# Kernel tuning notes

Measured on AMD Instinct MI355X. Metric: run time of the kernel, lower is better.

## Reference

```python
import jax, jax.numpy as jnp
import numpy as np
from jax import lax

BATCH, C, HH, WW = 4, 3, 512, 512


def _dark_min(x, patch):
    # min over channels, reflect-pad, min over patch x patch window (torch unfold+min)
    pad = (patch - 1) // 2
    m = jnp.min(x, axis=1, keepdims=True)                      # [B,1,H,W]
    m = jnp.pad(m, ((0, 0), (0, 0), (pad, pad), (pad, pad)), mode='reflect')
    return lax.reduce_window(m, jnp.array(jnp.inf, m.dtype), lax.min,
                             (1, 1, patch, patch), (1, 1, 1, 1), 'VALID')


def _soft_thresh(x, lam):
    return jnp.sign(x) * jnp.maximum(jnp.abs(x) - lam, 0.0)


def _conv3x3(x, w):
    return lax.conv_general_dilated(x, w, (1, 1), 'SAME',
                                    dimension_numbers=('NCHW', 'OIHW', 'NCHW'))


def setup_inputs() -> dict:
    key = jax.random.key(0)
    names = ['I', 't_p', 'B_p', 'B', 't', 'J', 'G', 'H', 'P', 'Q', 'u', 'v', 'X', 'Y']
    keys = jax.random.split(key, len(names) + 2)
    inp = {n: jax.random.uniform(keys[i], (BATCH, C, HH, WW), dtype=jnp.float32)
           for i, n in enumerate(names)}
    for g in ['gamma_1', 'gamma_2', 'gamma_3', 'gamma_4', 'gamma_5']:
        inp[g] = jnp.array([3.001], dtype=jnp.float32)
    inp['t1d_w'] = jax.random.normal(keys[-2], (1, 3, 1, 1), dtype=jnp.float32) * 0.3
    inp['hnet_w'] = jax.random.normal(keys[-1], (3, 3, 3, 3), dtype=jnp.float32) * 0.1
    inp['patch_size'] = 35
    return inp


def _forward(I, t_p, B_p, B, t, J, G, H, P, Q, u, v, X, Y,
             gamma_1, gamma_2, gamma_3, gamma_4, gamma_5, t1d_w, hnet_w, patch_size):
    lam1, lam2, lam3, lam4, lam5 = 1.0, 0.7, 0.3, 1.0, 1.0

    # ---- get_mean_value + mapping_index (vectorized over batch) ----
    mean = jnp.mean(J, axis=(2, 3))                 # [B,3]
    idx = jnp.argsort(mean, axis=1)                 # ascending, like torch.sort
    ms = jnp.take_along_axis(mean, idx, axis=1)     # sorted means
    gather = lambda k: jnp.take_along_axis(J, idx[:, k][:, None, None, None], axis=1)
    J_l, J_m, J_s = gather(2), gather(1), gather(0)           # [B,1,H,W]
    bar = lambda k: ms[:, k][:, None, None, None]
    J_m = J_m + (bar(2) - bar(1)) * J_l
    J_s = J_s + (bar(2) - bar(0)) * J_l
    ch = jnp.arange(3)[None, :]                     # scatter channels back
    J = jnp.where((ch == idx[:, 1:2])[:, :, None, None], J_m, J)
    J = jnp.where((ch == idx[:, 0:1])[:, :, None, None], J_s, J)

    # ---- B update (spatial mean broadcast back) ----
    Bn = (lam3 * B_p - lam1 * (J * t - I) * (1.0 - t)) / (lam1 * (1.0 - t) ** 2 + lam3)
    Bn = jnp.mean(Bn, axis=(2, 3), keepdims=True) * jnp.ones_like(I)

    # ---- t update + 1x1 conv + channel replicate ----
    tn = (lam2 * t_p + gamma_4 * H - lam1 * (Bn - I) * (J - Bn) - X) / \
         (lam1 * (J - Bn) ** 2 + lam2 + gamma_4)
    t1 = jnp.einsum('oc,bchw->bohw', t1d_w[:, :, 0, 0], tn)   # [B,1,H,W]
    tn = jnp.concatenate([t1, t1, t1], axis=1)

    # ---- J, u, v updates ----
    Jn = (lam1 * (tn * (I - Bn * (1.0 - tn))) + gamma_3 * G + gamma_4 * u
          - gamma_5 * v - Y + gamma_5) / (lam1 * tn * tn + gamma_3 + gamma_4 + gamma_5)
    un = (gamma_1 * u + gamma_4 * Jn) / (gamma_1 + gamma_4)
    vn = (gamma_2 * v - gamma_5 * Jn + gamma_5) / (gamma_2 + gamma_5)

    # ---- H_Net (conv stand-in for RDN), dual updates ----
    Hn = _conv3x3(tn + X / gamma_4, hnet_w)
    Xn = X + gamma_4 * (tn - Hn)
    Yn = Y + gamma_3 * (Jn - G)

    # ---- dark channel + soft threshold ----
    M_u = _dark_min(un, patch_size)
    M_v = _dark_min(vn, patch_size)
    Pn = _soft_thresh(M_u, lam4 / gamma_1)
    Qn = _soft_thresh(M_v, lam5 / gamma_1)

    return (Bn, tn, Jn, G, Hn, Pn, Qn, un, vn, Xn, Yn, gamma_3)


def reference(I, t_p, B_p, B, t, J, G, H, P, Q, u, v, X, Y,
              gamma_1, gamma_2, gamma_3, gamma_4, gamma_5, t1d_w, hnet_w, patch_size):
    return _forward(I, t_p, B_p, B, t, J, G, H, P, Q, u, v, X, Y,
                    gamma_1, gamma_2, gamma_3, gamma_4, gamma_5, t1d_w, hnet_w, patch_size)
```

## Files before the change

### kernel.cpp

```cpp
#include <hip/hip_runtime.h>
#include <math.h>

#define W_ 512
#define H_ 512
#define HW_ 262144
#define HW4_ 65536
#define CHW_ 786432

#define O_Bn 0
#define O_tn 3145728
#define O_Jn 6291456
#define O_G  9437184
#define O_Hn 12582912
#define O_Pn 15728640
#define O_Qn 16777216
#define O_un 17825792
#define O_vn 20971520
#define O_Xn 24117248
#define O_Yn 27262976
#define O_g3 30408704

#define LAM2 0.7f
#define LAM3 0.3f

#define WS_SUMS   0
#define WS_ALPHA  8192
#define WS_IDX2   8204
#define WS_BNS    8208
#define WS_SCR    16384

typedef float nfloat4 __attribute__((ext_vector_type(4)));

__device__ __forceinline__ void nt_store4(float4 v, float4* p) {
    nfloat4 nv; nv.x = v.x; nv.y = v.y; nv.z = v.z; nv.w = v.w;
    __builtin_nontemporal_store(nv, (nfloat4*)p);
}

__global__ __launch_bounds__(256) void kRed(const float* __restrict__ J,
                                            const float* __restrict__ tt,
                                            const float* __restrict__ B_p,
                                            const float* __restrict__ I,
                                            float* __restrict__ sums) {
    int blk = blockIdx.x;
    int b = blk >> 7, chunk = blk & 127;
    size_t pb = (size_t)b * (CHW_ / 4);
    size_t cb = (size_t)chunk * 512;
    const float4* J4 = (const float4*)J;
    const float4* t4 = (const float4*)tt;
    const float4* B4 = (const float4*)B_p;
    const float4* I4 = (const float4*)I;

    float aJ[3] = {0.f, 0.f, 0.f};
    float a1[3] = {0.f, 0.f, 0.f};
    float a2[9] = {0.f, 0.f, 0.f, 0.f, 0.f, 0.f, 0.f, 0.f, 0.f};

    #pragma unroll
    for (int k = 0; k < 2; ++k) {
        size_t o = cb + threadIdx.x + k * 256;
        float4 j0 = J4[pb + 0 * HW4_ + o];
        float4 j1 = J4[pb + 1 * HW4_ + o];
        float4 j2 = J4[pb + 2 * HW4_ + o];
        #pragma unroll
        for (int c = 0; c < 3; ++c) {
            float4 tv = t4[pb + (size_t)c * HW4_ + o];
            float4 bp = B4[pb + (size_t)c * HW4_ + o];
            float4 iv = I4[pb + (size_t)c * HW4_ + o];
            float4 jc = (c == 0) ? j0 : (c == 1 ? j1 : j2);
#define REDC(m) { \
            float omt = 1.f - tv.m; \
            float r = 1.f / (omt * omt + LAM3); \
            float g = tv.m * omt * r; \
            aJ[c] += jc.m; \
            a1[c] += (LAM3 * bp.m - (jc.m * tv.m - iv.m) * omt) * r; \
            a2[0 * 3 + c] += j0.m * g; \
            a2[1 * 3 + c] += j1.m * g; \
            a2[2 * 3 + c] += j2.m * g; }
            REDC(x) REDC(y) REDC(z) REDC(w)
#undef REDC
        }
    }

    float vals[15];
    #pragma unroll
    for (int c = 0; c < 3; ++c) { vals[c] = aJ[c]; vals[3 + c] = a1[c]; }
    #pragma unroll
    for (int s = 0; s < 9; ++s) vals[6 + s] = a2[s];

    __shared__ float lds[4][15];
    int lane = threadIdx.x & 63, w = threadIdx.x >> 6;
    #pragma unroll
    for (int s = 0; s < 15; ++s) {
        float v = vals[s];
        #pragma unroll
        for (int off = 32; off; off >>= 1) v += __shfl_down(v, off, 64);
        if (lane == 0) lds[w][s] = v;
    }
    __syncthreads();
    if (threadIdx.x < 15) {
        int s = threadIdx.x;
        sums[blk * 16 + s] = lds[0][s] + lds[1][s] + lds[2][s] + lds[3][s];
    }
}

__global__ __launch_bounds__(256) void kFin(const float* __restrict__ sums,
                     float* __restrict__ alpha, int* __restrict__ idx2,
                     float* __restrict__ BnS,
                     const float* __restrict__ g3p, float* __restrict__ outg3) {
    __shared__ float part[64][4];
    __shared__ float tot[4][15];
    int t = threadIdx.x;
    int g = t >> 2, sub = t & 3;
    if (g < 60) {
        int b = g / 15, s = g % 15;
        const float* p = sums + (size_t)b * 128 * 16 + s;
        float acc = 0.f;
        #pragma unroll 8
        for (int ch = sub; ch < 128; ch += 4) acc += p[ch * 16];
        part[g][sub] = acc;
    }
    __syncthreads();
    if (t < 60) {
        tot[t / 15][t % 15] = (part[t][0] + part[t][1]) + (part[t][2] + part[t][3]);
    }
    __syncthreads();
    if (t < 4) {
        const float invHW = 1.0f / (float)HW_;
        float m[3] = {tot[t][0] * invHW, tot[t][1] * invHW, tot[t][2] * invHW};
        int r[3];
        #pragma unroll
        for (int i = 0; i < 3; ++i) {
            int ri = 0;
            #pragma unroll
            for (int j = 0; j < 3; ++j)
                if (j != i && (m[j] < m[i] || (m[j] == m[i] && j < i))) ri++;
            r[i] = ri;
        }
        int idx[3]; float ms[3];
        #pragma unroll
        for (int i = 0; i < 3; ++i) { idx[r[i]] = i; ms[r[i]] = m[i]; }
        idx2[t] = idx[2];
        float a[3] = {0.f, 0.f, 0.f};
        a[idx[1]] = ms[2] - ms[1];
        a[idx[0]] = ms[2] - ms[0];
        #pragma unroll
        for (int c = 0; c < 3; ++c) {
            alpha[t * 3 + c] = a[c];
            BnS[t * 3 + c] = (tot[t][3 + c] - a[c] * tot[t][6 + idx[2] * 3 + c]) * invHW;
        }
    }
    if (t == 0) *outg3 = g3p[0];
}

__global__ __launch_bounds__(256) void kMain(
    const float* __restrict__ I, const float* __restrict__ t_p,
    const float* __restrict__ Hm, const float* __restrict__ Xm,
    const float* __restrict__ J, const float* __restrict__ u,
    const float* __restrict__ v, const float* __restrict__ Y,
    const float* __restrict__ G,
    const float* __restrict__ g1p, const float* __restrict__ g2p,
    const float* __restrict__ g3p, const float* __restrict__ g4p,
    const float* __restrict__ g5p, const float* __restrict__ t1w,
    const float* __restrict__ alpha, const int* __restrict__ idx2,
    const float* __restrict__ BnS,
    float* __restrict__ out)
{
    int id = blockIdx.x * 256 + threadIdx.x;
    int b = id >> 16, q = id & (HW4_ - 1);
    float g1 = g1p[0], g2 = g2p[0], g3 = g3p[0], g4 = g4p[0], g5 = g5p[0];
    float wc[3] = {t1w[0], t1w[1], t1w[2]};
    int i2 = idx2[b];
    size_t pb = (size_t)b * (CHW_ / 4);
    const float4* I4p = (const float4*)I;
    const float4* tp4p = (const float4*)t_p;
    const float4* H4p = (const float4*)Hm;
    const float4* X4p = (const float4*)Xm;
    const float4* J4p = (const float4*)J;
    const float4* u4p = (const float4*)u;
    const float4* v4p = (const float4*)v;
    const float4* Y4p = (const float4*)Y;
    const float4* G4p = (const float4*)G;
    float4* o4 = (float4*)out;

    float4 Jl = J4p[pb + (size_t)i2 * HW4_ + q];
    float4 t1 = make_float4(0.f, 0.f, 0.f, 0.f);
    float4 Isv[3]; float Bsv[3];
    const float den2 = LAM2 + g4;
    #pragma unroll
    for (int c = 0; c < 3; ++c) {
        size_t o = pb + (size_t)c * HW4_ + q;
        float4 I4 = I4p[o], tp4 = tp4p[o], H4 = H4p[o], X4 = X4p[o], Jv = J4p[o];
        float al = alpha[b * 3 + c], Bnv = BnS[b * 3 + c];
        float wcc = wc[c];
#define STEP1(m) { \
        float d_ = (Jv.m + al * Jl.m) - Bnv; \
        float tnr_ = (LAM2 * tp4.m + g4 * H4.m - (Bnv - I4.m) * d_ - X4.m) / (d_ * d_ + den2); \
        t1.m += wcc * tnr_; }
        STEP1(x) STEP1(y) STEP1(z) STEP1(w)
#undef STEP1
        Isv[c] = I4; Bsv[c] = Bnv;
    }
    float g345 = g3 + g4 + g5;
    float4 invDen;
    invDen.x = 1.f / (t1.x * t1.x + g345);
    invDen.y = 1.f / (t1.y * t1.y + g345);
    invDen.z = 1.f / (t1.z * t1.z + g345);
    invDen.w = 1.f / (t1.w * t1.w + g345);
    float invDu = 1.f / (g1 + g4), invDv = 1.f / (g2 + g5);
    float4 cu = make_float4(1e30f, 1e30f, 1e30f, 1e30f);
    float4 cv = cu;
    #pragma unroll
    for (int c = 0; c < 3; ++c) {
        size_t o = pb + (size_t)c * HW4_ + q;
        float4 u4 = u4p[o], v4 = v4p[o], Y4 = Y4p[o], G4 = G4p[o];
        float Bnv = Bsv[c];
        float4 Jn4, un4, vn4, Yn4;
#define STEP2(m) { \
        float Jn_ = (t1.m * (Isv[c].m - Bnv * (1.f - t1.m)) + g3 * G4.m + g4 * u4.m \
                     - g5 * v4.m - Y4.m + g5) * invDen.m; \
        float un_ = (g1 * u4.m + g4 * Jn_) * invDu; \
        float vn_ = (g2 * v4.m - g5 * Jn_ + g5) * invDv; \
        Jn4.m = Jn_; un4.m = un_; vn4.m = vn_; \
        Yn4.m = Y4.m + g3 * (Jn_ - G4.m); \
        cu.m = fminf(cu.m, un_); cv.m = fminf(cv.m, vn_); }
        STEP2(x) STEP2(y) STEP2(z) STEP2(w)
#undef STEP2
        nt_store4(make_float4(Bnv, Bnv, Bnv, Bnv), &o4[O_Bn / 4 + o]);
        o4[O_tn / 4 + o] = t1;
        nt_store4(Jn4, &o4[O_Jn / 4 + o]);
        nt_store4(G4,  &o4[O_G  / 4 + o]);
        nt_store4(un4, &o4[O_un / 4 + o]);
        nt_store4(vn4, &o4[O_vn / 4 + o]);
        nt_store4(Yn4, &o4[O_Yn / 4 + o]);
    }
    o4[O_Pn / 4 + (size_t)b * HW4_ + q] = cu;
    o4[O_Qn / 4 + (size_t)b * HW4_ + q] = cv;
}

__global__ __launch_bounds__(256) void kHMin(const float* __restrict__ out,
                                             float* __restrict__ scr) {
    __shared__ float row[546];
    int blk = blockIdx.x;
    int tensor = blk >> 11;
    int rem = blk & 2047;
    int b = rem >> 9, y = rem & 511;
    const float* src = out + (tensor ? O_Qn : O_Pn) + b * HW_ + y * W_;
    float* dst = scr + (size_t)(tensor * 4 + b) * HW_ + y * W_;
    for (int j = threadIdx.x; j < 546; j += 256) {
        int xx = j - 17;
        xx = xx < 0 ? -xx : (xx >= W_ ? 2 * W_ - 2 - xx : xx);
        row[j] = src[xx];
    }
    __syncthreads();
    for (int x = threadIdx.x; x < W_; x += 256) {
        float m = row[x];
        #pragma unroll
        for (int k = 1; k < 35; ++k) m = fminf(m, row[x + k]);
        dst[x] = m;
    }
}

__global__ __launch_bounds__(256) void kTail(const float* __restrict__ scr,
                                             const float* __restrict__ Xm,
                                             const float* __restrict__ hw,
                                             const float* __restrict__ g1p,
                                             const float* __restrict__ g4p,
                                             float* __restrict__ out) {
    __shared__ float w[81];
    if (blockIdx.x < 8192) {
        int tensor = blockIdx.x >> 12;
        int lid = ((blockIdx.x & 4095) << 8) + threadIdx.x;
        int b = lid >> 18, p = lid & (HW_ - 1);
        int y = p >> 9, x = p & 511;
        const float* R = scr + (size_t)(tensor * 4 + b) * HW_;
        float m = 1e30f;
        #pragma unroll
        for (int k = 0; k < 35; ++k) {
            int yy = y + k - 17;
            yy = yy < 0 ? -yy : (yy >= H_ ? 2 * H_ - 2 - yy : yy);
            m = fminf(m, R[yy * W_ + x]);
        }
        float lam = 1.0f / g1p[0];
        float s = (m > 0.f) ? 1.f : (m < 0.f ? -1.f : 0.f);
        float r = s * fmaxf(fabsf(m) - lam, 0.f);
        __builtin_nontemporal_store(r, &out[(tensor ? O_Qn : O_Pn) + b * HW_ + p]);
    } else {
        if (threadIdx.x < 81) w[threadIdx.x] = hw[threadIdx.x];
        __syncthreads();
        int id = (blockIdx.x - 8192) * 256 + threadIdx.x;
        int b = id >> 18, p = id & (HW_ - 1);
        int y = p >> 9, x = p & 511;
        float g4 = g4p[0], ig4 = 1.f / g4;
        const float* tn = out + O_tn + (size_t)b * CHW_;
        float acc0 = 0.f, acc1 = 0.f, acc2 = 0.f;
        #pragma unroll
        for (int ky = 0; ky < 3; ++ky) {
            int yy = y + ky - 1;
            if (yy < 0 || yy >= H_) continue;
            #pragma unroll
            for (int kx = 0; kx < 3; ++kx) {
                int xx = x + kx - 1;
                if (xx < 0 || xx >= W_) continue;
                int pp = yy * W_ + xx;
                float t1v = tn[pp];
                #pragma unroll
                for (int i = 0; i < 3; ++i) {
                    float Av = t1v + Xm[(size_t)(b * 3 + i) * HW_ + pp] * ig4;
                    int kk = i * 9 + ky * 3 + kx;
                    acc0 += w[kk] * Av;
                    acc1 += w[27 + kk] * Av;
                    acc2 += w[54 + kk] * Av;
                }
            }
        }
        float t1c = tn[p];
        float acc[3] = {acc0, acc1, acc2};
        #pragma unroll
        for (int o = 0; o < 3; ++o) {
            size_t oo = (size_t)(b * 3 + o) * HW_ + p;
            __builtin_nontemporal_store(acc[o], &out[O_Hn + oo]);
            __builtin_nontemporal_store(Xm[oo] + g4 * (t1c - acc[o]), &out[O_Xn + oo]);
        }
    }
}

extern "C" void kernel_launch(void* const* d_in, const int* in_sizes, int n_in,
                              void* d_out, int out_size, void* d_ws, size_t ws_size,
                              hipStream_t stream) {
    (void)in_sizes; (void)n_in; (void)out_size; (void)ws_size;
    const float* I   = (const float*)d_in[0];
    const float* t_p = (const float*)d_in[1];
    const float* B_p = (const float*)d_in[2];
    const float* tt  = (const float*)d_in[4];
    const float* J   = (const float*)d_in[5];
    const float* G   = (const float*)d_in[6];
    const float* Hm  = (const float*)d_in[7];
    const float* u   = (const float*)d_in[10];
    const float* v   = (const float*)d_in[11];
    const float* X   = (const float*)d_in[12];
    const float* Y   = (const float*)d_in[13];
    const float* g1  = (const float*)d_in[14];
    const float* g2  = (const float*)d_in[15];
    const float* g3  = (const float*)d_in[16];
    const float* g4  = (const float*)d_in[17];
    const float* g5  = (const float*)d_in[18];
    const float* t1w = (const float*)d_in[19];
    const float* hw  = (const float*)d_in[20];
    float* out = (float*)d_out;
    float* ws  = (float*)d_ws;

    float* sums  = ws + WS_SUMS;
    float* alpha = ws + WS_ALPHA;
    int*   idx2  = (int*)(ws + WS_IDX2);
    float* BnS   = ws + WS_BNS;
    float* scr   = ws + WS_SCR;

    kRed<<<512, 256, 0, stream>>>(J, tt, B_p, I, sums);
    kFin<<<1, 256, 0, stream>>>(sums, alpha, idx2, BnS, g3, out + O_g3);
    kMain<<<1024, 256, 0, stream>>>(I, t_p, Hm, X, J, u, v, Y, G,
                                    g1, g2, g3, g4, g5, t1w, alpha, idx2, BnS, out);
    kHMin<<<4096, 256, 0, stream>>>(out, scr);
    kTail<<<12288, 256, 0, stream>>>(scr, X, hw, g1, g4, out);
}
```

Before: 322.7 us.

## Fuse horizontal min into main kernel and tile 3x3 conv through LDS

Folds the horizontal 35-wide min pass into kMain: each block writes its two rows of channel-min values to shared memory, fills in the reflect padding and writes horizontal mins straight to scratch. This removes the kHMin launch and the write and re-read of the unfiltered Pn/Qn values. The tail kernel now does the vertical min with float4 loads, and computes the 3x3 conv from an LDS tile of (tn + X/g4) rows shared across output channels. Xn is rewritten as g4*(A - Hn), which is algebraically equal to the original. A leftover dead kTail stub remains in the source, and the kMain fusion assumes each 256-thread block covers exactly two full image rows.

```diff
diff --git a/kernel.cpp b/kernel.cpp
--- a/kernel.cpp
+++ b/kernel.cpp
@@ -162,8 +162,10 @@
     const float* __restrict__ g5p, const float* __restrict__ t1w,
     const float* __restrict__ alpha, const int* __restrict__ idx2,
     const float* __restrict__ BnS,
-    float* __restrict__ out)
+    float* __restrict__ out, float* __restrict__ scr)
 {
+    __shared__ float pad[2][2][560];
+
     int id = blockIdx.x * 256 + threadIdx.x;
     int b = id >> 16, q = id & (HW4_ - 1);
     float g1 = g1p[0], g2 = g2p[0], g3 = g3p[0], g4 = g4p[0], g5 = g5p[0];
@@ -232,93 +234,206 @@
         nt_store4(vn4, &o4[O_vn / 4 + o]);
         nt_store4(Yn4, &o4[O_Yn / 4 + o]);
     }
-    o4[O_Pn / 4 + (size_t)b * HW4_ + q] = cu;
-    o4[O_Qn / 4 + (size_t)b * HW4_ + q] = cv;
-}
-
-__global__ __launch_bounds__(256) void kHMin(const float* __restrict__ out,
-                                             float* __restrict__ scr) {
-    __shared__ float row[546];
-    int blk = blockIdx.x;
-    int tensor = blk >> 11;
-    int rem = blk & 2047;
-    int b = rem >> 9, y = rem & 511;
-    const float* src = out + (tensor ? O_Qn : O_Pn) + b * HW_ + y * W_;
-    float* dst = scr + (size_t)(tensor * 4 + b) * HW_ + y * W_;
-    for (int j = threadIdx.x; j < 546; j += 256) {
-        int xx = j - 17;
-        xx = xx < 0 ? -xx : (xx >= W_ ? 2 * W_ - 2 - xx : xx);
-        row[j] = src[xx];
-    }
+
+    int t = threadIdx.x;
+    int rrow = t >> 7;
+    int x0 = (t & 127) * 4;
+    pad[0][rrow][17 + x0 + 0] = cu.x;
+    pad[0][rrow][17 + x0 + 1] = cu.y;
+    pad[0][rrow][17 + x0 + 2] = cu.z;
+    pad[0][rrow][17 + x0 + 3] = cu.w;
+    pad[1][rrow][17 + x0 + 0] = cv.x;
+    pad[1][rrow][17 + x0 + 1] = cv.y;
+    pad[1][rrow][17 + x0 + 2] = cv.z;
+    pad[1][rrow][17 + x0 + 3] = cv.w;
     __syncthreads();
-    for (int x = threadIdx.x; x < W_; x += 256) {
-        float m = row[x];
-        #pragma unroll
-        for (int k = 1; k < 35; ++k) m = fminf(m, row[x + k]);
-        dst[x] = m;
+    if (t < 136) {
+        int which = t / 34, e = t % 34;
+        int tens = which >> 1, rw = which & 1;
+        int j   = (e < 17) ? e : (529 + (e - 17));
+        int src = (e < 17) ? (34 - j) : (1056 - j);
+        pad[tens][rw][j] = pad[tens][rw][src];
+    }
+    __syncthreads();
+
+    int y0b = (blockIdx.x & 255) * 2;
+    int yg = y0b + rrow;
+    #pragma unroll
+    for (int tens = 0; tens < 2; ++tens) {
+        const float* rowp = &pad[tens][rrow][0];
+        const float4* rp4 = (const float4*)(rowp + x0);
+        float4 qv = rp4[0];
+        float a0 = qv.x, a1 = qv.y, a2 = qv.z;
+        float mc = qv.w;
+        #pragma unroll
+        for (int i = 1; i < 8; ++i) {
+            qv = rp4[i];
+            mc = fminf(mc, fminf(fminf(qv.x, qv.y), fminf(qv.z, qv.w)));
+        }
+        qv = rp4[8];
+        mc = fminf(mc, fminf(qv.x, fminf(qv.y, qv.z)));
+        float a35 = qv.w;
+        qv = rp4[9];
+        float a36 = qv.x, a37 = qv.y;
+        float4 r;
+        r.x = fminf(fminf(a0, a1), fminf(a2, mc));
+        r.y = fminf(fminf(a1, a2), fminf(mc, a35));
+        r.z = fminf(fminf(a2, mc), fminf(a35, a36));
+        r.w = fminf(fminf(mc, a35), fminf(a36, a37));
+        *(float4*)(scr + (size_t)(tens * 4 + b) * HW_ + yg * W_ + x0) = r;
     }
 }
 
 __global__ __launch_bounds__(256) void kTail(const float* __restrict__ scr,
-                                             const float* __restrict__ Xm,
                                              const float* __restrict__ hw,
                                              const float* __restrict__ g1p,
                                              const float* __restrict__ g4p,
                                              float* __restrict__ out) {
-    __shared__ float w[81];
-    if (blockIdx.x < 8192) {
-        int tensor = blockIdx.x >> 12;
-        int lid = ((blockIdx.x & 4095) << 8) + threadIdx.x;
-        int b = lid >> 18, p = lid & (HW_ - 1);
-        int y = p >> 9, x = p & 511;
+    __shared__ float A_lds[3][4][528];
+    __shared__ float wsh[81];
+    int t = threadIdx.x;
+
+    if (blockIdx.x < 2048) {
+        int tensor = blockIdx.x >> 10;
+        int lid = ((blockIdx.x & 1023) << 8) + t;
+        int b = lid >> 16, qq = lid & (HW4_ - 1);
+        int y = qq >> 7, xq = (qq & 127) << 2;
         const float* R = scr + (size_t)(tensor * 4 + b) * HW_;
-        float m = 1e30f;
+        float4 m = make_float4(1e30f, 1e30f, 1e30f, 1e30f);
         #pragma unroll
         for (int k = 0; k < 35; ++k) {
             int yy = y + k - 17;
             yy = yy < 0 ? -yy : (yy >= H_ ? 2 * H_ - 2 - yy : yy);
-            m = fminf(m, R[yy * W_ + x]);
+            float4 r4 = *(const float4*)(R + yy * W_ + xq);
+            m.x = fminf(m.x, r4.x); m.y = fminf(m.y, r4.y);
+            m.z = fminf(m.z, r4.z); m.w = fminf(m.w, r4.w);
         }
         float lam = 1.0f / g1p[0];
-        float s = (m > 0.f) ? 1.f : (m < 0.f ? -1.f : 0.f);
-        float r = s * fmaxf(fabsf(m) - lam, 0.f);
-        __builtin_nontemporal_store(r, &out[(tensor ? O_Qn : O_Pn) + b * HW_ + p]);
+        float4 r;
+#define SOFT(m_, r_) { float s = (m_ > 0.f) ? 1.f : (m_ < 0.f ? -1.f : 0.f); \
+                       r_ = s * fmaxf(fabsf(m_) - lam, 0.f); }
+        SOFT(m.x, r.x) SOFT(m.y, r.y) SOFT(m.z, r.z) SOFT(m.w, r.w)
+#undef SOFT
+        nt_store4(r, (float4*)(out + (tensor ? O_Qn : O_Pn) + b * HW_ + y * W_ + xq));
     } else {
-        if (threadIdx.x < 81) w[threadIdx.x] = hw[threadIdx.x];
+        int cblk = blockIdx.x - 2048;
+        int b = cblk >> 8;
+        int y0 = (cblk & 255) * 2;
+        float g4 = g4p[0], ig4 = 1.f / g4;
+        const float* tn0 = out + O_tn + (size_t)b * CHW_;
+        const float* Xb  = out + O_Xn;
+        (void)Xb;
+        if (t < 81) wsh[t] = hw[t];
+        #pragma unroll
+        for (int k = 0; k < 6; ++k) {
+            int g = t + 256 * k;
+            int i = g >> 9, r = (g >> 7) & 3, xq = (g & 127) << 2;
+            int yy = y0 - 1 + r;
+            float4 A4;
+            if (yy >= 0 && yy < H_) {
+                const float* Xrow =  nullptr;
+                (void)Xrow;
+                A4 = make_float4(0.f, 0.f, 0.f, 0.f);
+            }
+            (void)A4; (void)i; (void)r; (void)xq; (void)yy;
+        }
+    }
+}
+
+__global__ __launch_bounds__(256) void kTail2(const float* __restrict__ scr,
+                                              const float* __restrict__ Xm,
+                                              const float* __restrict__ hw,
+                                              const float* __restrict__ g1p,
+                                              const float* __restrict__ g4p,
+                                              float* __restrict__ out) {
+    __shared__ float A_lds[3][4][528];
+    __shared__ float wsh[81];
+    int t = threadIdx.x;
+
+    if (blockIdx.x < 2048) {
+        int tensor = blockIdx.x >> 10;
+        int lid = ((blockIdx.x & 1023) << 8) + t;
+        int b = lid >> 16, qq = lid & (HW4_ - 1);
+        int y = qq >> 7, xq = (qq & 127) << 2;
+        const float* R = scr + (size_t)(tensor * 4 + b) * HW_;
+        float4 m = make_float4(1e30f, 1e30f, 1e30f, 1e30f);
+        #pragma unroll
+        for (int k = 0; k < 35; ++k) {
+            int yy = y + k - 17;
+            yy = yy < 0 ? -yy : (yy >= H_ ? 2 * H_ - 2 - yy : yy);
+            float4 r4 = *(const float4*)(R + yy * W_ + xq);
+            m.x = fminf(m.x, r4.x); m.y = fminf(m.y, r4.y);
+            m.z = fminf(m.z, r4.z); m.w = fminf(m.w, r4.w);
+        }
+        float lam = 1.0f / g1p[0];
+        float4 r;
+#define SOFT(m_, r_) { float s = (m_ > 0.f) ? 1.f : (m_ < 0.f ? -1.f : 0.f); \
+                       r_ = s * fmaxf(fabsf(m_) - lam, 0.f); }
+        SOFT(m.x, r.x) SOFT(m.y, r.y) SOFT(m.z, r.z) SOFT(m.w, r.w)
+#undef SOFT
+        nt_store4(r, (float4*)(out + (tensor ? O_Qn : O_Pn) + b * HW_ + y * W_ + xq));
+    } else {
+        int cblk = blockIdx.x - 2048;
+        int b = cblk >> 8;
+        int y0 = (cblk & 255) * 2;
+        float g4 = g4p[0], ig4 = 1.f / g4;
+        const float* tn0 = out + O_tn + (size_t)b * CHW_;
+        if (t < 81) wsh[t] = hw[t];
+        #pragma unroll
+        for (int k = 0; k < 6; ++k) {
+            int g = t + 256 * k;
+            int i = g >> 9, r = (g >> 7) & 3, xq = (g & 127) << 2;
+            int yy = y0 - 1 + r;
+            float4 A4 = make_float4(0.f, 0.f, 0.f, 0.f);
+            if (yy >= 0 && yy < H_) {
+                float4 tn4 = *(const float4*)(tn0 + yy * W_ + xq);
+                float4 X4  = *(const float4*)(Xm + (size_t)(b * 3 + i) * HW_ + yy * W_ + xq);
+                A4.x = tn4.x + X4.x * ig4; A4.y = tn4.y + X4.y * ig4;
+                A4.z = tn4.z + X4.z * ig4; A4.w = tn4.w + X4.w * ig4;
+            }
+            *(float4*)(&A_lds[i][r][4 + xq]) = A4;
+        }
+        if (t < 24) {
+            int pair = t >> 1, side = t & 1;
+            A_lds[pair >> 2][pair & 3][side ? 516 : 3] = 0.f;
+        }
         __syncthreads();
-        int id = (blockIdx.x - 8192) * 256 + threadIdx.x;
-        int b = id >> 18, p = id & (HW_ - 1);
-        int y = p >> 9, x = p & 511;
-        float g4 = g4p[0], ig4 = 1.f / g4;
-        const float* tn = out + O_tn + (size_t)b * CHW_;
-        float acc0 = 0.f, acc1 = 0.f, acc2 = 0.f;
-        #pragma unroll
-        for (int ky = 0; ky < 3; ++ky) {
-            int yy = y + ky - 1;
-            if (yy < 0 || yy >= H_) continue;
+
+        int tl = t & 127, r_out = t >> 7;
+        float acc[3][4] = {{0.f,0.f,0.f,0.f},{0.f,0.f,0.f,0.f},{0.f,0.f,0.f,0.f}};
+        #pragma unroll
+        for (int i = 0; i < 3; ++i) {
             #pragma unroll
-            for (int kx = 0; kx < 3; ++kx) {
-                int xx = x + kx - 1;
-                if (xx < 0 || xx >= W_) continue;
-                int pp = yy * W_ + xx;
-                float t1v = tn[pp];
+            for (int ky = 0; ky < 3; ++ky) {
+                const float* Ar = &A_lds[i][r_out + ky][0];
+                const float* wp0 = &wsh[0 * 27 + i * 9 + ky * 3];
+                const float* wp1 = &wsh[1 * 27 + i * 9 + ky * 3];
+                const float* wp2 = &wsh[2 * 27 + i * 9 + ky * 3];
+                float w00 = wp0[0], w01 = wp0[1], w02 = wp0[2];
+                float w10 = wp1[0], w11 = wp1[1], w12 = wp1[2];
+                float w20 = wp2[0], w21 = wp2[1], w22 = wp2[2];
                 #pragma unroll
-                for (int i = 0; i < 3; ++i) {
-                    float Av = t1v + Xm[(size_t)(b * 3 + i) * HW_ + pp] * ig4;
-                    int kk = i * 9 + ky * 3 + kx;
-                    acc0 += w[kk] * Av;
-                    acc1 += w[27 + kk] * Av;
-                    acc2 += w[54 + kk] * Av;
+                for (int j = 0; j < 4; ++j) {
+                    int x = tl + 128 * j;
+                    float am = Ar[3 + x], a0 = Ar[4 + x], ap = Ar[5 + x];
+                    acc[0][j] += w00 * am + w01 * a0 + w02 * ap;
+                    acc[1][j] += w10 * am + w11 * a0 + w12 * ap;
+                    acc[2][j] += w20 * am + w21 * a0 + w22 * ap;
                 }
             }
         }
-        float t1c = tn[p];
-        float acc[3] = {acc0, acc1, acc2};
+        int yg = y0 + r_out;
         #pragma unroll
         for (int o = 0; o < 3; ++o) {
-            size_t oo = (size_t)(b * 3 + o) * HW_ + p;
-            __builtin_nontemporal_store(acc[o], &out[O_Hn + oo]);
-            __builtin_nontemporal_store(Xm[oo] + g4 * (t1c - acc[o]), &out[O_Xn + oo]);
+            #pragma unroll
+            for (int j = 0; j < 4; ++j) {
+                int x = tl + 128 * j;
+                size_t oo = (size_t)(b * 3 + o) * HW_ + yg * W_ + x;
+                float hn = acc[o][j];
+                float Ac = A_lds[o][r_out + 1][4 + x];
+                __builtin_nontemporal_store(hn, &out[O_Hn + oo]);
+                __builtin_nontemporal_store(g4 * (Ac - hn), &out[O_Xn + oo]);
+            }
         }
     }
 }
@@ -357,7 +472,7 @@
     kRed<<<512, 256, 0, stream>>>(J, tt, B_p, I, sums);
     kFin<<<1, 256, 0, stream>>>(sums, alpha, idx2, BnS, g3, out + O_g3);
     kMain<<<1024, 256, 0, stream>>>(I, t_p, Hm, X, J, u, v, Y, G,
-                                    g1, g2, g3, g4, g5, t1w, alpha, idx2, BnS, out);
-    kHMin<<<4096, 256, 0, stream>>>(out, scr);
-    kTail<<<12288, 256, 0, stream>>>(scr, X, hw, g1, g4, out);
-}
+                                    g1, g2, g3, g4, g5, t1w, alpha, idx2, BnS,
+                                    out, scr);
+    kTail2<<<3072, 256, 0, stream>>>(scr, X, hw, g1, g4, out);
+}
```

Measured after the change: 310.6 us. 1.04x faster.
